# Performance work log

Hardware: AMD Instinct MI355X
Metric: run time of the kernel (lower is better)

## Reference

```python
import jax, jax.numpy as jnp
import numpy as np

B, S, D, H = 4, 2048, 1024, 16
DK = D // H
SCALE = float(np.sqrt(DK))
NEG_INF = jnp.float32(-1e30)


def setup_inputs() -> dict:
    key = jax.random.key(0)
    ks = jax.random.split(key, 12)
    std = 1.0 / np.sqrt(D)
    def lin(k):
        kw, kb = jax.random.split(k)
        W = jax.random.uniform(kw, (D, D), jnp.float32, -std, std)
        b = jax.random.uniform(kb, (D,), jnp.float32, -std, std)
        return W, b
    Wq, bq = lin(ks[0]); Wk, bk = lin(ks[1]); Wv, bv = lin(ks[2]); Wo, bo = lin(ks[3])
    query = jax.random.normal(ks[4], (B, S, D), jnp.float32)
    key_t = jax.random.normal(ks[5], (B, S, D), jnp.float32)
    value = jax.random.normal(ks[6], (B, S, D), jnp.float32)
    # causal mask, broadcastable to [B,H,S,S]; positions where mask==0 are blocked
    mask = jnp.tril(jnp.ones((S, S), dtype=bool))[None, None]
    return {"query": query, "key": key_t, "value": value,
            "Wq": Wq, "bq": bq, "Wk": Wk, "bk": bk, "Wv": Wv, "bv": bv,
            "Wo": Wo, "bo": bo, "mask": mask}


def reference(query, key, value, Wq, bq, Wk, bk, Wv, bv, Wo, bo, mask):
    # projections: x @ W.T + b (torch nn.Linear convention)
    q = (query @ Wq.T + bq).reshape(B, S, H, DK).transpose(0, 2, 1, 3)  # [B,H,S,DK]
    k = (key @ Wk.T + bk).reshape(B, S, H, DK).transpose(0, 2, 1, 3)
    v = (value @ Wv.T + bv).reshape(B, S, H, DK).transpose(0, 2, 1, 3)
    scores = jnp.einsum('bhqd,bhkd->bhqk', q, k) / SCALE  # [B,H,S,S]
    scores = jnp.where(mask, scores, NEG_INF)
    attn = jax.nn.softmax(scores, axis=-1)
    # dropout is identity in eval / p used at train only; omitted (p treated as 0)
    context = jnp.einsum('bhqk,bhkd->bhqd', attn, v)  # [B,H,S,DK]
    context = context.transpose(0, 2, 1, 3).reshape(B, S, D)
    return context @ Wo.T + bo
```

## Files before the change

### kernel.cpp

```cpp
#include <hip/hip_runtime.h>
#include <hip/hip_bf16.h>
#include <cstdint>
#include <cstddef>


namespace {

constexpr int B  = 4;
constexpr int S  = 2048;
constexpr int D  = 1024;
constexpr int H  = 16;
constexpr int DK = 64;
constexpr int M  = B * S;
constexpr float LOG2E     = 1.44269504088896f;
constexpr float QSCALE    = 0.125f * LOG2E;
constexpr float NEG_BIG   = -1e30f;
constexpr float DEFER_THR = 8.0f;

using bf16 = __hip_bfloat16;

typedef __attribute__((ext_vector_type(8))) __bf16 bf16x8;
typedef __attribute__((ext_vector_type(4))) float  f32x4;

__device__ __forceinline__ uint16_t f2bfu(float x) {
  uint32_t a = __builtin_bit_cast(uint32_t, x);
  return (uint16_t)((a + 0x7FFFu + ((a >> 16) & 1u)) >> 16);
}
__device__ __forceinline__ uint32_t pk2(float x, float y) {
  return (uint32_t)f2bfu(x) | ((uint32_t)f2bfu(y) << 16);
}
__device__ __forceinline__ float ex2(float x) {
  float r; asm("v_exp_f32 %0, %1" : "=v"(r) : "v"(x)); return r;
}
__device__ __forceinline__ uint32_t cvtpk(float lo, float hi) {
  uint32_t r;
  asm("v_cvt_pk_bf16_f32 %0, %1, %2" : "=v"(r) : "v"(lo), "v"(hi));
  return r;
}
__device__ __forceinline__ float hmax4(f32x4 v) {
  return fmaxf(fmaxf(v[0], v[1]), fmaxf(v[2], v[3]));
}

__device__ __forceinline__ void ldst16(const uint4* g, uint4* l) {
  __builtin_amdgcn_global_load_lds(
      (const __attribute__((address_space(1))) void*)g,
      (__attribute__((address_space(3))) void*)l, 16, 0, 0);
}

__device__ __forceinline__ void xcd_remap(int& bx, int& by) {
  const int orig = blockIdx.x + (blockIdx.y << 3);
  bx = (orig >> 3) & 7;
  by = ((orig & 7) << 3) + (orig >> 6);
}

__global__ __launch_bounds__(256)
void cvt_all(const float* __restrict__ q, const float* __restrict__ k,
             const float* __restrict__ v, const float* __restrict__ wq,
             const float* __restrict__ wk, const float* __restrict__ wv,
             const float* __restrict__ wo, bf16* __restrict__ dq,
             bf16* __restrict__ dk, bf16* __restrict__ dv,
             bf16* __restrict__ dw)
{
  constexpr int N8IN = 1 << 20;
  constexpr int N8W  = 1 << 17;
  constexpr int T3   = 3 * N8IN;

  const int gi = blockIdx.x * 256 + threadIdx.x;
  const float* src; bf16* dst; int i;
  if (gi < T3) {
    const int z = gi >> 20; i = gi & (N8IN - 1);
    src = (z == 0) ? q : (z == 1) ? k : v;
    dst = (z == 0) ? dq : (z == 1) ? dk : dv;
  } else {
    const int j = gi - T3;
    const int z = j >> 17; i = j & (N8W - 1);
    src = (z == 0) ? wq : (z == 1) ? wk : (z == 2) ? wv : wo;
    dst = dw + ((size_t)z << 20);
  }
  const float4 p = ((const float4*)src)[2 * i];
  const float4 r4 = ((const float4*)src)[2 * i + 1];
  uint4 r;
  r.x = pk2(p.x, p.y); r.y = pk2(p.z, p.w);
  r.z = pk2(r4.x, r4.y); r.w = pk2(r4.z, r4.w);
  ((uint4*)dst)[i] = r;
}

__global__ __launch_bounds__(256)
void cvt3(const float* __restrict__ a, const float* __restrict__ b,
          const float* __restrict__ c, bf16* __restrict__ x,
          bf16* __restrict__ y, bf16* __restrict__ z_, int n8)
{
  const int zz = blockIdx.y;
  const float* src = (zz == 0) ? a : (zz == 1) ? b : c;
  bf16*        dst = (zz == 0) ? x : (zz == 1) ? y : z_;
  const int i = blockIdx.x * 256 + threadIdx.x;
  if (i >= n8) return;
  const float4 p = ((const float4*)src)[2 * i];
  const float4 q = ((const float4*)src)[2 * i + 1];
  uint4 r;
  r.x = pk2(p.x, p.y); r.y = pk2(p.z, p.w);
  r.z = pk2(q.x, q.y); r.w = pk2(q.z, q.w);
  ((uint4*)dst)[i] = r;
}

__global__ __launch_bounds__(256, 4)
void proj_qkv(const bf16* __restrict__ Aq, const bf16* __restrict__ Ak,
              const bf16* __restrict__ Av, const bf16* __restrict__ Wall,
              const float* __restrict__ bq_, const float* __restrict__ bk_,
              const float* __restrict__ bv_, bf16* __restrict__ qo,
              bf16* __restrict__ ko, bf16* __restrict__ vto)
{
  __shared__ uint4 AsU[1024];
  __shared__ uint4 BsU[1024];

  const int z = blockIdx.z;
  const bf16*  A    = (z == 0) ? Aq : (z == 1) ? Ak : Av;
  const bf16*  Wb   = Wall + (size_t)z * D * D;
  const float* bias = (z == 0) ? bq_ : (z == 1) ? bk_ : bv_;

  const int tid  = threadIdx.x;
  const int w    = tid >> 6;
  const int lane = tid & 63;
  const int lm   = lane & 15;
  const int quad = lane >> 4;
  const int wm   = (w >> 1) * 64;
  const int wn   = (w & 1) * 64;

  int bx, by; xcd_remap(bx, by);
  const int row0 = by * 128, col0 = bx * 128;
  constexpr int g8 = D >> 3;

  const uint4* Ag = (const uint4*)A + (size_t)row0 * g8;
  const uint4* Bg = (const uint4*)Wb + (size_t)col0 * g8;

  f32x4 acc[4][4] = {};

  for (int kt = 0; kt < D / 64; ++kt) {
    __syncthreads();
#pragma unroll
    for (int i = 0; i < 4; ++i) {
      const int chunk = i * 256 + w * 64 + lane;
      const int r = chunk >> 3, c = chunk & 7;
      ldst16(&Ag[(size_t)r * g8 + kt * 8 + c], &AsU[i * 256 + w * 64]);
      ldst16(&Bg[(size_t)r * g8 + kt * 8 + c], &BsU[i * 256 + w * 64]);
    }
    __syncthreads();
#pragma unroll
    for (int kk = 0; kk < 2; ++kk) {
      bf16x8 af[4], bfr[4];
#pragma unroll
      for (int tm = 0; tm < 4; ++tm)
        af[tm] = __builtin_bit_cast(bf16x8, AsU[(wm + tm * 16 + lm) * 8 + kk * 4 + quad]);
#pragma unroll
      for (int tn = 0; tn < 4; ++tn)
        bfr[tn] = __builtin_bit_cast(bf16x8, BsU[(wn + tn * 16 + lm) * 8 + kk * 4 + quad]);
#pragma unroll
      for (int tm = 0; tm < 4; ++tm)
#pragma unroll
        for (int tn = 0; tn < 4; ++tn)
          acc[tm][tn] = __builtin_amdgcn_mfma_f32_16x16x32_bf16(af[tm], bfr[tn], acc[tm][tn], 0, 0, 0);
    }
  }

  const float scale = (z == 0) ? QSCALE : 1.0f;
#pragma unroll
  for (int tm = 0; tm < 4; ++tm) {
#pragma unroll
    for (int tn = 0; tn < 4; ++tn) {
      const int col = col0 + wn + tn * 16 + lm;
      const float bv = bias[col];
      if (z == 2) {
        float vv[4];
#pragma unroll
        for (int r = 0; r < 4; ++r) vv[r] = acc[tm][tn][r] + bv;
        const int s0 = row0 + wm + tm * 16 + quad * 4;
        const int b_ = s0 >> 11, ss = s0 & (S - 1);
        const int h_ = col >> 6, dk = col & (DK - 1);
        uint2 st; st.x = pk2(vv[0], vv[1]); st.y = pk2(vv[2], vv[3]);
        *(uint2*)(vto + (((size_t)b_ * H + h_) * DK + dk) * S + ss) = st;
      } else {
        bf16* out = (z == 0) ? qo : ko;
#pragma unroll
        for (int r = 0; r < 4; ++r) {
          const int row = row0 + wm + tm * 16 + quad * 4 + r;
          const float v = (acc[tm][tn][r] + bv) * scale;
          const int b_ = row >> 11, s_ = row & (S - 1);
          const int h_ = col >> 6,  dk = col & (DK - 1);
          out[(((size_t)b_ * H + h_) * S + s_) * DK + dk] =
              __builtin_bit_cast(bf16, f2bfu(v));
        }
      }
    }
  }
}

__global__ __launch_bounds__(512)
void gemm_out(const bf16* __restrict__ A, const bf16* __restrict__ Wb,
              const float* __restrict__ bias, float* __restrict__ out)
{
  __shared__ uint4 AsU[1024];
  __shared__ uint4 BsU[1024];

  const int tid  = threadIdx.x;
  const int w    = tid >> 6;
  const int lane = tid & 63;
  const int lm   = lane & 15;
  const int quad = lane >> 4;
  const int wm   = (w >> 2) * 64;
  const int wn   = (w & 3) * 32;

  int bx, by; xcd_remap(bx, by);
  const int row0 = by * 128, col0 = bx * 128;
  constexpr int g8 = D >> 3;

  const uint4* Ag = (const uint4*)A + (size_t)row0 * g8;
  const uint4* Bg = (const uint4*)Wb + (size_t)col0 * g8;

  f32x4 acc[4][2] = {};

  for (int kt = 0; kt < D / 64; ++kt) {
    __syncthreads();
#pragma unroll
    for (int i = 0; i < 2; ++i) {
      const int chunk = i * 512 + w * 64 + lane;
      const int r = chunk >> 3, c = chunk & 7;
      ldst16(&Ag[(size_t)r * g8 + kt * 8 + c], &AsU[i * 512 + w * 64]);
      ldst16(&Bg[(size_t)r * g8 + kt * 8 + c], &BsU[i * 512 + w * 64]);
    }
    __syncthreads();
#pragma unroll
    for (int kk = 0; kk < 2; ++kk) {
      bf16x8 af[4], bfr[2];
#pragma unroll
      for (int tm = 0; tm < 4; ++tm)
        af[tm] = __builtin_bit_cast(bf16x8, AsU[(wm + tm * 16 + lm) * 8 + kk * 4 + quad]);
#pragma unroll
      for (int tn = 0; tn < 2; ++tn)
        bfr[tn] = __builtin_bit_cast(bf16x8, BsU[(wn + tn * 16 + lm) * 8 + kk * 4 + quad]);
#pragma unroll
      for (int tm = 0; tm < 4; ++tm)
#pragma unroll
        for (int tn = 0; tn < 2; ++tn)
          acc[tm][tn] = __builtin_amdgcn_mfma_f32_16x16x32_bf16(af[tm], bfr[tn], acc[tm][tn], 0, 0, 0);
    }
  }

#pragma unroll
  for (int tm = 0; tm < 4; ++tm) {
#pragma unroll
    for (int tn = 0; tn < 2; ++tn) {
      const int col = col0 + wn + tn * 16 + lm;
      const float bv = bias[col];
#pragma unroll
      for (int r = 0; r < 4; ++r) {
        const int row = row0 + wm + tm * 16 + quad * 4 + r;
        out[(size_t)row * D + col] = acc[tm][tn][r] + bv;
      }
    }
  }
}

template <int MODE>
__global__ __launch_bounds__(256)
void gemm128(const bf16* __restrict__ A, const bf16* __restrict__ Wb,
             const float* __restrict__ bias, void* __restrict__ out,
             int N, int K, float scale)
{
  __shared__ uint4 AsU[2][1024];
  __shared__ uint4 BsU[2][1024];

  const int tid  = threadIdx.x;
  const int w    = tid >> 6;
  const int lane = tid & 63;
  const int lm   = lane & 15;
  const int quad = lane >> 4;
  const int wm   = (w >> 1) * 64;
  const int wn   = (w & 1) * 64;

  int bx, by; xcd_remap(bx, by);
  const int row0 = by * 128, col0 = bx * 128;
  const int g8 = K >> 3;

  const uint4* Ag = (const uint4*)A + (size_t)row0 * g8;
  const uint4* Bg = (const uint4*)Wb + (size_t)col0 * g8;

  f32x4 acc[4][4] = {};
  const int KT = K / 64;

#pragma unroll
  for (int i = 0; i < 4; ++i) {
    const int chunk = i * 256 + w * 64 + lane;
    const int r = chunk >> 3, c = chunk & 7;
    ldst16(&Ag[(size_t)r * g8 + c], &AsU[0][i * 256 + w * 64]);
    ldst16(&Bg[(size_t)r * g8 + c], &BsU[0][i * 256 + w * 64]);
  }

  int cur = 0;
  for (int kt = 0; kt < KT; ++kt) {
    __syncthreads();
    if (kt + 1 < KT) {
#pragma unroll
      for (int i = 0; i < 4; ++i) {
        const int chunk = i * 256 + w * 64 + lane;
        const int r = chunk >> 3, c = chunk & 7;
        ldst16(&Ag[(size_t)r * g8 + (kt + 1) * 8 + c], &AsU[cur ^ 1][i * 256 + w * 64]);
        ldst16(&Bg[(size_t)r * g8 + (kt + 1) * 8 + c], &BsU[cur ^ 1][i * 256 + w * 64]);
      }
    }
#pragma unroll
    for (int kk = 0; kk < 2; ++kk) {
      bf16x8 af[4], bfr[4];
#pragma unroll
      for (int tm = 0; tm < 4; ++tm)
        af[tm] = __builtin_bit_cast(bf16x8, AsU[cur][(wm + tm * 16 + lm) * 8 + kk * 4 + quad]);
#pragma unroll
      for (int tn = 0; tn < 4; ++tn)
        bfr[tn] = __builtin_bit_cast(bf16x8, BsU[cur][(wn + tn * 16 + lm) * 8 + kk * 4 + quad]);
#pragma unroll
      for (int tm = 0; tm < 4; ++tm)
#pragma unroll
        for (int tn = 0; tn < 4; ++tn)
          acc[tm][tn] = __builtin_amdgcn_mfma_f32_16x16x32_bf16(af[tm], bfr[tn], acc[tm][tn], 0, 0, 0);
    }
    cur ^= 1;
  }

#pragma unroll
  for (int tm = 0; tm < 4; ++tm) {
#pragma unroll
    for (int tn = 0; tn < 4; ++tn) {
      const int col = col0 + wn + tn * 16 + lm;
      const float bv = bias[col];
      if (MODE == 2) {
        float vv[4];
#pragma unroll
        for (int r = 0; r < 4; ++r) vv[r] = (acc[tm][tn][r] + bv) * scale;
        const int s0 = row0 + wm + tm * 16 + quad * 4;
        const int b_ = s0 >> 11, ss = s0 & (S - 1);
        const int h_ = col >> 6, dk = col & (DK - 1);
        uint2 st; st.x = pk2(vv[0], vv[1]); st.y = pk2(vv[2], vv[3]);
        *(uint2*)((bf16*)out + (((size_t)b_ * H + h_) * DK + dk) * S + ss) = st;
      } else {
#pragma unroll
        for (int r = 0; r < 4; ++r) {
          const int row = row0 + wm + tm * 16 + quad * 4 + r;
          const float v = (acc[tm][tn][r] + bv) * scale;
          if (MODE == 0) {
            ((float*)out)[(size_t)row * N + col] = v;
          } else {
            const int b_ = row >> 11, s_ = row & (S - 1);
            const int h_ = col >> 6,  dk = col & (DK - 1);
            ((bf16*)out)[(((size_t)b_ * H + h_) * S + s_) * DK + dk] =
                __builtin_bit_cast(bf16, f2bfu(v));
          }
        }
      }
    }
  }
}

__global__ __launch_bounds__(512)
void flash_mfma(const bf16* __restrict__ Q, const bf16* __restrict__ K,
                const bf16* __restrict__ Vt, bf16* __restrict__ ctx)
{
  __shared__ uint4 KsU[2][512];
  __shared__ uint4 VtU[2][512];
  __shared__ uint16_t Os[128 * 72];

  const int tid  = threadIdx.x;
  const int w    = tid >> 6;
  const int lane = tid & 63;
  const int lm   = lane & 15;
  const int quad = lane >> 4;
  const int bh   = blockIdx.x;
  const int pr   = blockIdx.y;
  const size_t base = (size_t)bh * S * DK;

  const uint4* Kg0 = (const uint4*)(K + base);
  const uint4* Vg0 = (const uint4*)(Vt + (size_t)bh * DK * S);

  const int rr  = w * 8 + (lane >> 3);
  const int csw = (lane & 7) ^ (lane >> 3) ^ ((w & 1) << 2);
  const int fv  = (lm & 7) ^ (((lm >> 3) & 1) << 2);
  const int r0  = ((lm >> 2) << 3) | (lm & 3);

  uint16_t* const Ow = Os + (w * 16) * 72;
  const int b_ = bh >> 4, h_ = bh & (H - 1);

  for (int pass = 0; pass < 2; ++pass) {
    const int qi = pass ? (15 - pr) : pr;
    const int q0 = qi * 128;
    const int qbase = q0 + w * 16;

    bf16x8 qf0, qf1;
    {
      const bf16* qrow = Q + base + (size_t)(qbase + lm) * DK;
      qf0 = __builtin_bit_cast(bf16x8, *(const uint4*)(qrow + quad * 8));
      qf1 = __builtin_bit_cast(bf16x8, *(const uint4*)(qrow + 32 + quad * 8));
    }

    f32x4 o[4] = {};
    float m_i = NEG_BIG, l_i = 0.f;

    const int nt = 2 * qi + 2;

    ldst16(&Kg0[(size_t)rr * 8 + csw],       &KsU[0][w * 64]);
    ldst16(&Vg0[(size_t)rr * (S / 8) + csw], &VtU[0][w * 64]);

    int cur = 0;
    for (int t = 0; t < nt; ++t) {
      __syncthreads();
      if (t + 1 < nt) {
        const int k1 = (t + 1) * 64;
        ldst16(&Kg0[(size_t)(k1 + rr) * 8 + csw],         &KsU[cur ^ 1][w * 64]);
        ldst16(&Vg0[(size_t)rr * (S / 8) + k1 / 8 + csw], &VtU[cur ^ 1][w * 64]);
      }
      const int k0 = t * 64;
      if (k0 <= qbase + 15) {
        const uint4* Ks = KsU[cur];
        const uint4* Vs = VtU[cur];

        f32x4 sc[4];
        __builtin_amdgcn_s_setprio(1);
#pragma unroll
        for (int tn = 0; tn < 4; ++tn) {
          const int row = r0 + ((tn & 1) << 2) + ((tn >> 1) << 5);
          const int fr  = (row & 7) ^ (((row >> 3) & 1) << 2);
          const int cb  = quad ^ fr;
          bf16x8 kb0 = __builtin_bit_cast(bf16x8, Ks[row * 8 + cb]);
          bf16x8 kb1 = __builtin_bit_cast(bf16x8, Ks[row * 8 + (cb ^ 4)]);
          sc[tn] = __builtin_amdgcn_mfma_f32_16x16x32_bf16(
                       kb0, qf0, f32x4{0.f, 0.f, 0.f, 0.f}, 0, 0, 0);
          sc[tn] = __builtin_amdgcn_mfma_f32_16x16x32_bf16(kb1, qf1, sc[tn], 0, 0, 0);
        }
        __builtin_amdgcn_s_setprio(0);

        if (k0 + 63 > qbase) {
          const int qg = qbase + lm;
#pragma unroll
          for (int tn = 0; tn < 4; ++tn) {
            const int kb_ = k0 + ((tn >> 1) << 5) + (quad << 3) + ((tn & 1) << 2);
#pragma unroll
            for (int r = 0; r < 4; ++r)
              if (kb_ + r > qg) sc[tn][r] = NEG_BIG;
          }
        }

        float mloc = fmaxf(fmaxf(hmax4(sc[0]), hmax4(sc[1])),
                           fmaxf(hmax4(sc[2]), hmax4(sc[3])));
        mloc = fmaxf(mloc, __shfl_xor(mloc, 16));
        mloc = fmaxf(mloc, __shfl_xor(mloc, 32));

        if (__any(mloc > m_i + DEFER_THR)) {
          const float mn = fmaxf(m_i, mloc);
          const float al = ex2(m_i - mn);
          l_i *= al; m_i = mn;
          const float a0 = __shfl(al, quad * 4 + 0, 16);
          const float a1 = __shfl(al, quad * 4 + 1, 16);
          const float a2 = __shfl(al, quad * 4 + 2, 16);
          const float a3 = __shfl(al, quad * 4 + 3, 16);
#pragma unroll
          for (int tn = 0; tn < 4; ++tn) {
            o[tn][0] *= a0; o[tn][1] *= a1; o[tn][2] *= a2; o[tn][3] *= a3;
          }
        }

        float ls = 0.f;
#pragma unroll
        for (int tn = 0; tn < 4; ++tn) {
#pragma unroll
          for (int r = 0; r < 4; ++r) sc[tn][r] = ex2(sc[tn][r] - m_i);
          ls += (sc[tn][0] + sc[tn][1]) + (sc[tn][2] + sc[tn][3]);
        }
        l_i += ls;

        uint4 pw0, pw1;
        pw0.x = cvtpk(sc[0][0], sc[0][1]); pw0.y = cvtpk(sc[0][2], sc[0][3]);
        pw0.z = cvtpk(sc[1][0], sc[1][1]); pw0.w = cvtpk(sc[1][2], sc[1][3]);
        pw1.x = cvtpk(sc[2][0], sc[2][1]); pw1.y = cvtpk(sc[2][2], sc[2][3]);
        pw1.z = cvtpk(sc[3][0], sc[3][1]); pw1.w = cvtpk(sc[3][2], sc[3][3]);
        const bf16x8 ap0 = __builtin_bit_cast(bf16x8, pw0);
        const bf16x8 ap1 = __builtin_bit_cast(bf16x8, pw1);

        __builtin_amdgcn_s_setprio(1);
#pragma unroll
        for (int tn = 0; tn < 4; ++tn) {
          const int vrow = tn * 16 + lm;
          const int cv = quad ^ fv;
          bf16x8 vb0 = __builtin_bit_cast(bf16x8, Vs[vrow * 8 + cv]);
          bf16x8 vb1 = __builtin_bit_cast(bf16x8, Vs[vrow * 8 + (cv ^ 4)]);
          o[tn] = __builtin_amdgcn_mfma_f32_16x16x32_bf16(ap0, vb0, o[tn], 0, 0, 0);
          o[tn] = __builtin_amdgcn_mfma_f32_16x16x32_bf16(ap1, vb1, o[tn], 0, 0, 0);
        }
        __builtin_amdgcn_s_setprio(0);
      }
      cur ^= 1;
    }

    __syncthreads();
    {
      float lr = l_i;
      lr += __shfl_xor(lr, 16);
      lr += __shfl_xor(lr, 32);
      const float inv = 1.f / lr;
      const float i0 = __shfl(inv, quad * 4 + 0, 16);
      const float i1 = __shfl(inv, quad * 4 + 1, 16);
      const float i2 = __shfl(inv, quad * 4 + 2, 16);
      const float i3 = __shfl(inv, quad * 4 + 3, 16);
#pragma unroll
      for (int tn = 0; tn < 4; ++tn) {
        Ow[(quad * 4 + 0) * 72 + tn * 16 + lm] = f2bfu(o[tn][0] * i0);
        Ow[(quad * 4 + 1) * 72 + tn * 16 + lm] = f2bfu(o[tn][1] * i1);
        Ow[(quad * 4 + 2) * 72 + tn * 16 + lm] = f2bfu(o[tn][2] * i2);
        Ow[(quad * 4 + 3) * 72 + tn * 16 + lm] = f2bfu(o[tn][3] * i3);
      }
    }
    __syncthreads();

#pragma unroll
    for (int i = 0; i < 2; ++i) {
      const int idx = tid + i * 512;
      const int row = idx >> 3, c = idx & 7;
      const uint4 v = *(const uint4*)(Os + row * 72 + c * 8);
      *(uint4*)(ctx + ((((size_t)b_ * S + q0 + row) * H + h_) << 6) + c * 8) = v;
    }
  }
}

}

extern "C" void kernel_launch(void* const* d_in, const int* in_sizes, int n_in,
                              void* d_out, int out_size, void* d_ws, size_t ws_size,
                              hipStream_t stream)
{
  const float* query = (const float*)d_in[0];
  const float* key_  = (const float*)d_in[1];
  const float* value = (const float*)d_in[2];
  const float* Wq    = (const float*)d_in[3];
  const float* bq    = (const float*)d_in[4];
  const float* Wk    = (const float*)d_in[5];
  const float* bk    = (const float*)d_in[6];
  const float* Wv    = (const float*)d_in[7];
  const float* bv    = (const float*)d_in[8];
  const float* Wo    = (const float*)d_in[9];
  const float* bo    = (const float*)d_in[10];

  const size_t qkv = (size_t)B * H * S * DK;
  const size_t DD  = (size_t)D * D;
  bf16* slot0 = (bf16*)d_ws;
  bf16* slot1 = slot0 + qkv;
  bf16* slot2 = slot1 + qkv;
  bf16* slot3 = slot2 + qkv;
  bf16* slot4 = slot3 + qkv;
  bf16* dout0 = (bf16*)d_out;
  bf16* dout1 = dout0 + qkv;

  const int n8in = (int)(qkv / 8);
  const int n8w  = (int)(DD / 8);
  const dim3 gproj(D / 128, M / 128);
  const dim3 gattn(B * H, 8);

  const size_t need = (4 * qkv + 4 * DD) * sizeof(bf16);

  if (ws_size >= need) {
    cvt_all<<<dim3((3 * n8in + 4 * n8w) / 256), 256, 0, stream>>>(
        query, key_, value, Wq, Wk, Wv, Wo, dout0, dout1, slot3, slot4);
    proj_qkv<<<dim3(D / 128, M / 128, 3), 256, 0, stream>>>(
        dout0, dout1, slot3, slot4, bq, bk, bv, slot0, slot1, slot2);
    flash_mfma<<<gattn, 512, 0, stream>>>(slot0, slot1, slot2, slot3);
    gemm_out<<<gproj, 512, 0, stream>>>(slot3, slot4 + 3 * DD, bo,
                                        (float*)d_out);
  } else {
    cvt3<<<dim3(n8in / 256, 3), 256, 0, stream>>>(query, key_, value,
                                                  dout0, dout1, slot3, n8in);
    cvt3<<<dim3(n8w / 256, 2), 256, 0, stream>>>(Wq, Wk, Wk,
                                                 slot2, slot2 + DD, slot2, n8w);
    gemm128<1><<<gproj, 256, 0, stream>>>(dout0, slot2, bq, slot0, D, D, QSCALE);
    gemm128<1><<<gproj, 256, 0, stream>>>(dout1, slot2 + DD, bk, slot1, D, D, 1.0f);
    cvt3<<<dim3(n8w / 256, 1), 256, 0, stream>>>(Wv, Wv, Wv,
                                                 dout0, dout0, dout0, n8w);
    gemm128<2><<<gproj, 256, 0, stream>>>(slot3, dout0, bv, slot2, D, D, 1.0f);
    flash_mfma<<<gattn, 512, 0, stream>>>(slot0, slot1, slot2, slot3);
    cvt3<<<dim3(n8w / 256, 1), 256, 0, stream>>>(Wo, Wo, Wo,
                                                 slot0, slot0, slot0, n8w);
    gemm128<0><<<gproj, 256, 0, stream>>>(slot3, slot0, bo, d_out, D, D, 1.0f);
  }
}
```

Baseline: 315.7 us.

## Pipeline projection GEMMs with triple-buffered LDS and 256x128 tiles

Rewrites the QKV projection and output GEMMs to use 256x128 block tiles with 512 threads and a three-stage LDS ring fed by async global-to-LDS loads, so the next tiles load while the current one computes. It XOR-swizzles the LDS layout to avoid bank conflicts, raises MFMA priority with setprio, and remaps blocks across XCDs for the new grid shape. The cost is much larger shared memory (144KB per block), which limits occupancy to one block per CU, and halves the number of blocks.

Result: slower. 325.9 us (+3.2%).

```diff
diff --git a/kernel.cpp b/kernel.cpp
--- a/kernel.cpp
+++ b/kernel.cpp
@@ -51,6 +51,13 @@
   const int orig = blockIdx.x + (blockIdx.y << 3);
   bx = (orig >> 3) & 7;
   by = ((orig & 7) << 3) + (orig >> 6);
+}
+
+__device__ __forceinline__ void xcd_remap256(int& bx, int& by) {
+  const int d = blockIdx.x + (blockIdx.y << 3);
+  const int j = d >> 3;
+  bx = j >> 2;
+  by = ((d & 7) << 2) | (j & 3);
 }
 
 __global__ __launch_bounds__(256)
@@ -103,15 +110,72 @@
   ((uint4*)dst)[i] = r;
 }
 
-__global__ __launch_bounds__(256, 4)
-void proj_qkv(const bf16* __restrict__ Aq, const bf16* __restrict__ Ak,
-              const bf16* __restrict__ Av, const bf16* __restrict__ Wall,
-              const float* __restrict__ bq_, const float* __restrict__ bk_,
-              const float* __restrict__ bv_, bf16* __restrict__ qo,
-              bf16* __restrict__ ko, bf16* __restrict__ vto)
+
+#define PIPE_STAGE(T, SL)                                                     \
+  {                                                                           \
+    const int kb = (T) * 8;                                                   \
+    _Pragma("unroll")                                                         \
+    for (int i = 0; i < 4; ++i)                                               \
+      ldst16(&Ag[(size_t)(i * 64 + rr) * 128 + kb + cs],                      \
+             &As[SL][i * 512 + (w << 6)]);                                    \
+    _Pragma("unroll")                                                         \
+    for (int i = 0; i < 2; ++i)                                               \
+      ldst16(&Bg[(size_t)(i * 64 + rr) * 128 + kb + cs],                      \
+             &Bs[SL][i * 512 + (w << 6)]);                                    \
+  }
+
+#define PIPE_LOOP()                                                           \
+  PIPE_STAGE(0, 0);                                                           \
+  PIPE_STAGE(1, 1);                                                           \
+  int s = 0;                                                                  \
+  for (int t = 0; t < 16; ++t) {                                              \
+    if (t < 15) asm volatile("s_waitcnt vmcnt(6)" ::: "memory");              \
+    else        asm volatile("s_waitcnt vmcnt(0)" ::: "memory");              \
+    __builtin_amdgcn_s_barrier();                                             \
+    __builtin_amdgcn_sched_barrier(0);                                        \
+    if (t + 2 < 16) {                                                         \
+      int s2 = s + 2; if (s2 >= 3) s2 -= 3;                                   \
+      PIPE_STAGE(t + 2, s2);                                                  \
+    }                                                                         \
+    const uint4* Asl = As[s];                                                 \
+    const uint4* Bsl = Bs[s];                                                 \
+    _Pragma("unroll")                                                         \
+    for (int qd = 0; qd < 4; ++qd) {                                          \
+      const int tm0 = (qd >> 1) * 2, tn0 = (qd & 1) * 2;                      \
+      bf16x8 a0[2], a1[2], b0[2], b1[2];                                      \
+      _Pragma("unroll")                                                       \
+      for (int x = 0; x < 2; ++x) {                                           \
+        const int ra = (wm + (tm0 + x) * 16 + lm) * 8;                        \
+        a0[x] = __builtin_bit_cast(bf16x8, Asl[ra + kc0]);                    \
+        a1[x] = __builtin_bit_cast(bf16x8, Asl[ra + (kc0 ^ 4)]);              \
+        const int rb = (wn + (tn0 + x) * 16 + lm) * 8;                        \
+        b0[x] = __builtin_bit_cast(bf16x8, Bsl[rb + kc0]);                    \
+        b1[x] = __builtin_bit_cast(bf16x8, Bsl[rb + (kc0 ^ 4)]);              \
+      }                                                                       \
+      __builtin_amdgcn_s_setprio(1);                                          \
+      _Pragma("unroll")                                                       \
+      for (int x = 0; x < 2; ++x)                                             \
+        _Pragma("unroll")                                                     \
+        for (int y = 0; y < 2; ++y) {                                         \
+          acc[tm0 + x][tn0 + y] = __builtin_amdgcn_mfma_f32_16x16x32_bf16(    \
+              a0[x], b0[y], acc[tm0 + x][tn0 + y], 0, 0, 0);                  \
+          acc[tm0 + x][tn0 + y] = __builtin_amdgcn_mfma_f32_16x16x32_bf16(    \
+              a1[x], b1[y], acc[tm0 + x][tn0 + y], 0, 0, 0);                  \
+        }                                                                     \
+      __builtin_amdgcn_s_setprio(0);                                          \
+    }                                                                         \
+    ++s; if (s == 3) s = 0;                                                   \
+  }
+
+__global__ __launch_bounds__(512)
+void proj_qkv8(const bf16* __restrict__ Aq, const bf16* __restrict__ Ak,
+               const bf16* __restrict__ Av, const bf16* __restrict__ Wall,
+               const float* __restrict__ bq_, const float* __restrict__ bk_,
+               const float* __restrict__ bv_, bf16* __restrict__ qo,
+               bf16* __restrict__ ko, bf16* __restrict__ vto)
 {
-  __shared__ uint4 AsU[1024];
-  __shared__ uint4 BsU[1024];
+  __shared__ uint4 As[3][2048];
+  __shared__ uint4 Bs[3][1024];
 
   const int z = blockIdx.z;
   const bf16*  A    = (z == 0) ? Aq : (z == 1) ? Ak : Av;
@@ -126,41 +190,19 @@
   const int wm   = (w >> 1) * 64;
   const int wn   = (w & 1) * 64;
 
-  int bx, by; xcd_remap(bx, by);
-  const int row0 = by * 128, col0 = bx * 128;
-  constexpr int g8 = D >> 3;
-
-  const uint4* Ag = (const uint4*)A + (size_t)row0 * g8;
-  const uint4* Bg = (const uint4*)Wb + (size_t)col0 * g8;
+  int bx, by; xcd_remap256(bx, by);
+  const int row0 = by * 256, col0 = bx * 128;
+
+  const uint4* Ag = (const uint4*)A + (size_t)row0 * 128;
+  const uint4* Bg = (const uint4*)Wb + (size_t)col0 * 128;
+
+  const int rr = (w << 3) + (lane >> 3);
+  const int cs = (lane & 7) ^ (lane >> 3);
+  const int kc0 = quad ^ (lm & 7);
 
   f32x4 acc[4][4] = {};
 
-  for (int kt = 0; kt < D / 64; ++kt) {
-    __syncthreads();
-#pragma unroll
-    for (int i = 0; i < 4; ++i) {
-      const int chunk = i * 256 + w * 64 + lane;
-      const int r = chunk >> 3, c = chunk & 7;
-      ldst16(&Ag[(size_t)r * g8 + kt * 8 + c], &AsU[i * 256 + w * 64]);
-      ldst16(&Bg[(size_t)r * g8 + kt * 8 + c], &BsU[i * 256 + w * 64]);
-    }
-    __syncthreads();
-#pragma unroll
-    for (int kk = 0; kk < 2; ++kk) {
-      bf16x8 af[4], bfr[4];
-#pragma unroll
-      for (int tm = 0; tm < 4; ++tm)
-        af[tm] = __builtin_bit_cast(bf16x8, AsU[(wm + tm * 16 + lm) * 8 + kk * 4 + quad]);
-#pragma unroll
-      for (int tn = 0; tn < 4; ++tn)
-        bfr[tn] = __builtin_bit_cast(bf16x8, BsU[(wn + tn * 16 + lm) * 8 + kk * 4 + quad]);
-#pragma unroll
-      for (int tm = 0; tm < 4; ++tm)
-#pragma unroll
-        for (int tn = 0; tn < 4; ++tn)
-          acc[tm][tn] = __builtin_amdgcn_mfma_f32_16x16x32_bf16(af[tm], bfr[tn], acc[tm][tn], 0, 0, 0);
-    }
-  }
+  PIPE_LOOP();
 
   const float scale = (z == 0) ? QSCALE : 1.0f;
 #pragma unroll
@@ -195,60 +237,38 @@
 }
 
 __global__ __launch_bounds__(512)
-void gemm_out(const bf16* __restrict__ A, const bf16* __restrict__ Wb,
-              const float* __restrict__ bias, float* __restrict__ out)
+void gemm_out8(const bf16* __restrict__ A, const bf16* __restrict__ Wb,
+               const float* __restrict__ bias, float* __restrict__ out)
 {
-  __shared__ uint4 AsU[1024];
-  __shared__ uint4 BsU[1024];
+  __shared__ uint4 As[3][2048];
+  __shared__ uint4 Bs[3][1024];
 
   const int tid  = threadIdx.x;
   const int w    = tid >> 6;
   const int lane = tid & 63;
   const int lm   = lane & 15;
   const int quad = lane >> 4;
-  const int wm   = (w >> 2) * 64;
-  const int wn   = (w & 3) * 32;
-
-  int bx, by; xcd_remap(bx, by);
-  const int row0 = by * 128, col0 = bx * 128;
-  constexpr int g8 = D >> 3;
-
-  const uint4* Ag = (const uint4*)A + (size_t)row0 * g8;
-  const uint4* Bg = (const uint4*)Wb + (size_t)col0 * g8;
-
-  f32x4 acc[4][2] = {};
-
-  for (int kt = 0; kt < D / 64; ++kt) {
-    __syncthreads();
-#pragma unroll
-    for (int i = 0; i < 2; ++i) {
-      const int chunk = i * 512 + w * 64 + lane;
-      const int r = chunk >> 3, c = chunk & 7;
-      ldst16(&Ag[(size_t)r * g8 + kt * 8 + c], &AsU[i * 512 + w * 64]);
-      ldst16(&Bg[(size_t)r * g8 + kt * 8 + c], &BsU[i * 512 + w * 64]);
-    }
-    __syncthreads();
-#pragma unroll
-    for (int kk = 0; kk < 2; ++kk) {
-      bf16x8 af[4], bfr[2];
-#pragma unroll
-      for (int tm = 0; tm < 4; ++tm)
-        af[tm] = __builtin_bit_cast(bf16x8, AsU[(wm + tm * 16 + lm) * 8 + kk * 4 + quad]);
-#pragma unroll
-      for (int tn = 0; tn < 2; ++tn)
-        bfr[tn] = __builtin_bit_cast(bf16x8, BsU[(wn + tn * 16 + lm) * 8 + kk * 4 + quad]);
-#pragma unroll
-      for (int tm = 0; tm < 4; ++tm)
-#pragma unroll
-        for (int tn = 0; tn < 2; ++tn)
-          acc[tm][tn] = __builtin_amdgcn_mfma_f32_16x16x32_bf16(af[tm], bfr[tn], acc[tm][tn], 0, 0, 0);
-    }
-  }
+  const int wm   = (w >> 1) * 64;
+  const int wn   = (w & 1) * 64;
+
+  int bx, by; xcd_remap256(bx, by);
+  const int row0 = by * 256, col0 = bx * 128;
+
+  const uint4* Ag = (const uint4*)A + (size_t)row0 * 128;
+  const uint4* Bg = (const uint4*)Wb + (size_t)col0 * 128;
+
+  const int rr = (w << 3) + (lane >> 3);
+  const int cs = (lane & 7) ^ (lane >> 3);
+  const int kc0 = quad ^ (lm & 7);
+
+  f32x4 acc[4][4] = {};
+
+  PIPE_LOOP();
 
 #pragma unroll
   for (int tm = 0; tm < 4; ++tm) {
 #pragma unroll
-    for (int tn = 0; tn < 2; ++tn) {
+    for (int tn = 0; tn < 4; ++tn) {
       const int col = col0 + wn + tn * 16 + lm;
       const float bv = bias[col];
 #pragma unroll
@@ -565,11 +585,11 @@
   if (ws_size >= need) {
     cvt_all<<<dim3((3 * n8in + 4 * n8w) / 256), 256, 0, stream>>>(
         query, key_, value, Wq, Wk, Wv, Wo, dout0, dout1, slot3, slot4);
-    proj_qkv<<<dim3(D / 128, M / 128, 3), 256, 0, stream>>>(
+    proj_qkv8<<<dim3(8, 32, 3), 512, 0, stream>>>(
         dout0, dout1, slot3, slot4, bq, bk, bv, slot0, slot1, slot2);
     flash_mfma<<<gattn, 512, 0, stream>>>(slot0, slot1, slot2, slot3);
-    gemm_out<<<gproj, 512, 0, stream>>>(slot3, slot4 + 3 * DD, bo,
-                                        (float*)d_out);
+    gemm_out8<<<dim3(8, 32), 512, 0, stream>>>(slot3, slot4 + 3 * DD, bo,
+                                               (float*)d_out);
   } else {
     cvt3<<<dim3(n8in / 256, 3), 256, 0, stream>>>(query, key_, value,
                                                   dout0, dout1, slot3, n8in);
```

## Give each attention wave two 16-row query groups with 256-thread blocks

Applied to the files above, without the earlier changes.

The flash attention kernel drops from 8 waves of 16 query rows each to 4 waves of 32 query rows each (two 16-row groups per wave). Each K/V fragment read from LDS is now reused across two MFMA row groups, which halves LDS reads per unit of compute, and each thread issues twice as many global-to-LDS loads. The cost is doubled per-wave register state (two score tiles, two output accumulators, two softmax states) and fewer waves per block to hide latency. Causal skipping is kept per 16-row group.

After: 332.4 us. +5.3%, slower.

```diff
diff --git a/kernel.cpp b/kernel.cpp
--- a/kernel.cpp
+++ b/kernel.cpp
@@ -359,7 +359,7 @@
   }
 }
 
-__global__ __launch_bounds__(512)
+__global__ __launch_bounds__(256)
 void flash_mfma(const bf16* __restrict__ Q, const bf16* __restrict__ K,
                 const bf16* __restrict__ Vt, bf16* __restrict__ ctx)
 {
@@ -379,48 +379,54 @@
   const uint4* Kg0 = (const uint4*)(K + base);
   const uint4* Vg0 = (const uint4*)(Vt + (size_t)bh * DK * S);
 
-  const int rr  = w * 8 + (lane >> 3);
-  const int csw = (lane & 7) ^ (lane >> 3) ^ ((w & 1) << 2);
+  const int rr  = tid >> 3;
+  const int csw = (tid & 7) ^ ((tid >> 3) & 7) ^ (((tid >> 6) & 1) << 2);
   const int fv  = (lm & 7) ^ (((lm >> 3) & 1) << 2);
   const int r0  = ((lm >> 2) << 3) | (lm & 3);
 
-  uint16_t* const Ow = Os + (w * 16) * 72;
   const int b_ = bh >> 4, h_ = bh & (H - 1);
 
   for (int pass = 0; pass < 2; ++pass) {
     const int qi = pass ? (15 - pr) : pr;
     const int q0 = qi * 128;
-    const int qbase = q0 + w * 16;
-
-    bf16x8 qf0, qf1;
-    {
-      const bf16* qrow = Q + base + (size_t)(qbase + lm) * DK;
-      qf0 = __builtin_bit_cast(bf16x8, *(const uint4*)(qrow + quad * 8));
-      qf1 = __builtin_bit_cast(bf16x8, *(const uint4*)(qrow + 32 + quad * 8));
-    }
-
-    f32x4 o[4] = {};
-    float m_i = NEG_BIG, l_i = 0.f;
+    const int qb = q0 + w * 32;
+
+    bf16x8 qf[2][2];
+#pragma unroll
+    for (int g = 0; g < 2; ++g) {
+      const bf16* qrow = Q + base + (size_t)(qb + g * 16 + lm) * DK;
+      qf[g][0] = __builtin_bit_cast(bf16x8, *(const uint4*)(qrow + quad * 8));
+      qf[g][1] = __builtin_bit_cast(bf16x8, *(const uint4*)(qrow + 32 + quad * 8));
+    }
+
+    f32x4 o[2][4] = {};
+    float m_i[2] = {NEG_BIG, NEG_BIG};
+    float l_i[2] = {0.f, 0.f};
 
     const int nt = 2 * qi + 2;
 
-    ldst16(&Kg0[(size_t)rr * 8 + csw],       &KsU[0][w * 64]);
-    ldst16(&Vg0[(size_t)rr * (S / 8) + csw], &VtU[0][w * 64]);
+    ldst16(&Kg0[(size_t)rr * 8 + csw],               &KsU[0][w * 64]);
+    ldst16(&Kg0[(size_t)(32 + rr) * 8 + csw],        &KsU[0][256 + w * 64]);
+    ldst16(&Vg0[(size_t)rr * (S / 8) + csw],         &VtU[0][w * 64]);
+    ldst16(&Vg0[(size_t)(32 + rr) * (S / 8) + csw],  &VtU[0][256 + w * 64]);
 
     int cur = 0;
     for (int t = 0; t < nt; ++t) {
       __syncthreads();
       if (t + 1 < nt) {
         const int k1 = (t + 1) * 64;
-        ldst16(&Kg0[(size_t)(k1 + rr) * 8 + csw],         &KsU[cur ^ 1][w * 64]);
-        ldst16(&Vg0[(size_t)rr * (S / 8) + k1 / 8 + csw], &VtU[cur ^ 1][w * 64]);
+        ldst16(&Kg0[(size_t)(k1 + rr) * 8 + csw],               &KsU[cur ^ 1][w * 64]);
+        ldst16(&Kg0[(size_t)(k1 + 32 + rr) * 8 + csw],          &KsU[cur ^ 1][256 + w * 64]);
+        ldst16(&Vg0[(size_t)rr * (S / 8) + k1 / 8 + csw],       &VtU[cur ^ 1][w * 64]);
+        ldst16(&Vg0[(size_t)(32 + rr) * (S / 8) + k1 / 8 + csw], &VtU[cur ^ 1][256 + w * 64]);
       }
       const int k0 = t * 64;
-      if (k0 <= qbase + 15) {
+      if (k0 <= qb + 31) {
+        const bool a0 = (k0 <= qb + 15);
         const uint4* Ks = KsU[cur];
         const uint4* Vs = VtU[cur];
 
-        f32x4 sc[4];
+        f32x4 sc[2][4];
         __builtin_amdgcn_s_setprio(1);
 #pragma unroll
         for (int tn = 0; tn < 4; ++tn) {
@@ -429,58 +435,70 @@
           const int cb  = quad ^ fr;
           bf16x8 kb0 = __builtin_bit_cast(bf16x8, Ks[row * 8 + cb]);
           bf16x8 kb1 = __builtin_bit_cast(bf16x8, Ks[row * 8 + (cb ^ 4)]);
-          sc[tn] = __builtin_amdgcn_mfma_f32_16x16x32_bf16(
-                       kb0, qf0, f32x4{0.f, 0.f, 0.f, 0.f}, 0, 0, 0);
-          sc[tn] = __builtin_amdgcn_mfma_f32_16x16x32_bf16(kb1, qf1, sc[tn], 0, 0, 0);
+          sc[1][tn] = __builtin_amdgcn_mfma_f32_16x16x32_bf16(
+                          kb0, qf[1][0], f32x4{0.f, 0.f, 0.f, 0.f}, 0, 0, 0);
+          sc[1][tn] = __builtin_amdgcn_mfma_f32_16x16x32_bf16(kb1, qf[1][1], sc[1][tn], 0, 0, 0);
+          if (a0) {
+            sc[0][tn] = __builtin_amdgcn_mfma_f32_16x16x32_bf16(
+                            kb0, qf[0][0], f32x4{0.f, 0.f, 0.f, 0.f}, 0, 0, 0);
+            sc[0][tn] = __builtin_amdgcn_mfma_f32_16x16x32_bf16(kb1, qf[0][1], sc[0][tn], 0, 0, 0);
+          }
         }
         __builtin_amdgcn_s_setprio(0);
 
-        if (k0 + 63 > qbase) {
-          const int qg = qbase + lm;
+        bf16x8 ap[2][2];
+#pragma unroll
+        for (int g = 0; g < 2; ++g) {
+          if (g == 0 && !a0) continue;
+          const int qbg = qb + g * 16;
+          if (k0 + 63 > qbg) {
+            const int qg = qbg + lm;
+#pragma unroll
+            for (int tn = 0; tn < 4; ++tn) {
+              const int kb_ = k0 + ((tn >> 1) << 5) + (quad << 3) + ((tn & 1) << 2);
+#pragma unroll
+              for (int r = 0; r < 4; ++r)
+                if (kb_ + r > qg) sc[g][tn][r] = NEG_BIG;
+            }
+          }
+
+          float mloc = fmaxf(fmaxf(hmax4(sc[g][0]), hmax4(sc[g][1])),
+                             fmaxf(hmax4(sc[g][2]), hmax4(sc[g][3])));
+          mloc = fmaxf(mloc, __shfl_xor(mloc, 16));
+          mloc = fmaxf(mloc, __shfl_xor(mloc, 32));
+
+          if (__any(mloc > m_i[g] + DEFER_THR)) {
+            const float mn = fmaxf(m_i[g], mloc);
+            const float al = ex2(m_i[g] - mn);
+            l_i[g] *= al; m_i[g] = mn;
+            const float a0_ = __shfl(al, quad * 4 + 0, 16);
+            const float a1_ = __shfl(al, quad * 4 + 1, 16);
+            const float a2_ = __shfl(al, quad * 4 + 2, 16);
+            const float a3_ = __shfl(al, quad * 4 + 3, 16);
+#pragma unroll
+            for (int tn = 0; tn < 4; ++tn) {
+              o[g][tn][0] *= a0_; o[g][tn][1] *= a1_;
+              o[g][tn][2] *= a2_; o[g][tn][3] *= a3_;
+            }
+          }
+
+          float ls = 0.f;
 #pragma unroll
           for (int tn = 0; tn < 4; ++tn) {
-            const int kb_ = k0 + ((tn >> 1) << 5) + (quad << 3) + ((tn & 1) << 2);
-#pragma unroll
-            for (int r = 0; r < 4; ++r)
-              if (kb_ + r > qg) sc[tn][r] = NEG_BIG;
+#pragma unroll
+            for (int r = 0; r < 4; ++r) sc[g][tn][r] = ex2(sc[g][tn][r] - m_i[g]);
+            ls += (sc[g][tn][0] + sc[g][tn][1]) + (sc[g][tn][2] + sc[g][tn][3]);
           }
+          l_i[g] += ls;
+
+          uint4 pw0, pw1;
+          pw0.x = cvtpk(sc[g][0][0], sc[g][0][1]); pw0.y = cvtpk(sc[g][0][2], sc[g][0][3]);
+          pw0.z = cvtpk(sc[g][1][0], sc[g][1][1]); pw0.w = cvtpk(sc[g][1][2], sc[g][1][3]);
+          pw1.x = cvtpk(sc[g][2][0], sc[g][2][1]); pw1.y = cvtpk(sc[g][2][2], sc[g][2][3]);
+          pw1.z = cvtpk(sc[g][3][0], sc[g][3][1]); pw1.w = cvtpk(sc[g][3][2], sc[g][3][3]);
+          ap[g][0] = __builtin_bit_cast(bf16x8, pw0);
+          ap[g][1] = __builtin_bit_cast(bf16x8, pw1);
         }
-
-        float mloc = fmaxf(fmaxf(hmax4(sc[0]), hmax4(sc[1])),
-                           fmaxf(hmax4(sc[2]), hmax4(sc[3])));
-        mloc = fmaxf(mloc, __shfl_xor(mloc, 16));
-        mloc = fmaxf(mloc, __shfl_xor(mloc, 32));
-
-        if (__any(mloc > m_i + DEFER_THR)) {
-          const float mn = fmaxf(m_i, mloc);
-          const float al = ex2(m_i - mn);
-          l_i *= al; m_i = mn;
-          const float a0 = __shfl(al, quad * 4 + 0, 16);
-          const float a1 = __shfl(al, quad * 4 + 1, 16);
-          const float a2 = __shfl(al, quad * 4 + 2, 16);
-          const float a3 = __shfl(al, quad * 4 + 3, 16);
-#pragma unroll
-          for (int tn = 0; tn < 4; ++tn) {
-            o[tn][0] *= a0; o[tn][1] *= a1; o[tn][2] *= a2; o[tn][3] *= a3;
-          }
-        }
-
-        float ls = 0.f;
-#pragma unroll
-        for (int tn = 0; tn < 4; ++tn) {
-#pragma unroll
-          for (int r = 0; r < 4; ++r) sc[tn][r] = ex2(sc[tn][r] - m_i);
-          ls += (sc[tn][0] + sc[tn][1]) + (sc[tn][2] + sc[tn][3]);
-        }
-        l_i += ls;
-
-        uint4 pw0, pw1;
-        pw0.x = cvtpk(sc[0][0], sc[0][1]); pw0.y = cvtpk(sc[0][2], sc[0][3]);
-        pw0.z = cvtpk(sc[1][0], sc[1][1]); pw0.w = cvtpk(sc[1][2], sc[1][3]);
-        pw1.x = cvtpk(sc[2][0], sc[2][1]); pw1.y = cvtpk(sc[2][2], sc[2][3]);
-        pw1.z = cvtpk(sc[3][0], sc[3][1]); pw1.w = cvtpk(sc[3][2], sc[3][3]);
-        const bf16x8 ap0 = __builtin_bit_cast(bf16x8, pw0);
-        const bf16x8 ap1 = __builtin_bit_cast(bf16x8, pw1);
 
         __builtin_amdgcn_s_setprio(1);
 #pragma unroll
@@ -489,8 +507,12 @@
           const int cv = quad ^ fv;
           bf16x8 vb0 = __builtin_bit_cast(bf16x8, Vs[vrow * 8 + cv]);
           bf16x8 vb1 = __builtin_bit_cast(bf16x8, Vs[vrow * 8 + (cv ^ 4)]);
-          o[tn] = __builtin_amdgcn_mfma_f32_16x16x32_bf16(ap0, vb0, o[tn], 0, 0, 0);
-          o[tn] = __builtin_amdgcn_mfma_f32_16x16x32_bf16(ap1, vb1, o[tn], 0, 0, 0);
+          o[1][tn] = __builtin_amdgcn_mfma_f32_16x16x32_bf16(ap[1][0], vb0, o[1][tn], 0, 0, 0);
+          o[1][tn] = __builtin_amdgcn_mfma_f32_16x16x32_bf16(ap[1][1], vb1, o[1][tn], 0, 0, 0);
+          if (a0) {
+            o[0][tn] = __builtin_amdgcn_mfma_f32_16x16x32_bf16(ap[0][0], vb0, o[0][tn], 0, 0, 0);
+            o[0][tn] = __builtin_amdgcn_mfma_f32_16x16x32_bf16(ap[0][1], vb1, o[0][tn], 0, 0, 0);
+          }
         }
         __builtin_amdgcn_s_setprio(0);
       }
@@ -498,8 +520,10 @@
     }
 
     __syncthreads();
-    {
-      float lr = l_i;
+#pragma unroll
+    for (int g = 0; g < 2; ++g) {
+      uint16_t* const Ow = Os + (w * 32 + g * 16) * 72;
+      float lr = l_i[g];
       lr += __shfl_xor(lr, 16);
       lr += __shfl_xor(lr, 32);
       const float inv = 1.f / lr;
@@ -509,17 +533,17 @@
       const float i3 = __shfl(inv, quad * 4 + 3, 16);
 #pragma unroll
       for (int tn = 0; tn < 4; ++tn) {
-        Ow[(quad * 4 + 0) * 72 + tn * 16 + lm] = f2bfu(o[tn][0] * i0);
-        Ow[(quad * 4 + 1) * 72 + tn * 16 + lm] = f2bfu(o[tn][1] * i1);
-        Ow[(quad * 4 + 2) * 72 + tn * 16 + lm] = f2bfu(o[tn][2] * i2);
-        Ow[(quad * 4 + 3) * 72 + tn * 16 + lm] = f2bfu(o[tn][3] * i3);
+        Ow[(quad * 4 + 0) * 72 + tn * 16 + lm] = f2bfu(o[g][tn][0] * i0);
+        Ow[(quad * 4 + 1) * 72 + tn * 16 + lm] = f2bfu(o[g][tn][1] * i1);
+        Ow[(quad * 4 + 2) * 72 + tn * 16 + lm] = f2bfu(o[g][tn][2] * i2);
+        Ow[(quad * 4 + 3) * 72 + tn * 16 + lm] = f2bfu(o[g][tn][3] * i3);
       }
     }
     __syncthreads();
 
 #pragma unroll
-    for (int i = 0; i < 2; ++i) {
-      const int idx = tid + i * 512;
+    for (int i = 0; i < 4; ++i) {
+      const int idx = tid + i * 256;
       const int row = idx >> 3, c = idx & 7;
       const uint4 v = *(const uint4*)(Os + row * 72 + c * 8);
       *(uint4*)(ctx + ((((size_t)b_ * S + q0 + row) * H + h_) << 6) + c * 8) = v;
@@ -567,7 +591,7 @@
         query, key_, value, Wq, Wk, Wv, Wo, dout0, dout1, slot3, slot4);
     proj_qkv<<<dim3(D / 128, M / 128, 3), 256, 0, stream>>>(
         dout0, dout1, slot3, slot4, bq, bk, bv, slot0, slot1, slot2);
-    flash_mfma<<<gattn, 512, 0, stream>>>(slot0, slot1, slot2, slot3);
+    flash_mfma<<<gattn, 256, 0, stream>>>(slot0, slot1, slot2, slot3);
     gemm_out<<<gproj, 512, 0, stream>>>(slot3, slot4 + 3 * DD, bo,
                                         (float*)d_out);
   } else {
@@ -580,7 +604,7 @@
     cvt3<<<dim3(n8w / 256, 1), 256, 0, stream>>>(Wv, Wv, Wv,
                                                  dout0, dout0, dout0, n8w);
     gemm128<2><<<gproj, 256, 0, stream>>>(slot3, dout0, bv, slot2, D, D, 1.0f);
-    flash_mfma<<<gattn, 512, 0, stream>>>(slot0, slot1, slot2, slot3);
+    flash_mfma<<<gattn, 256, 0, stream>>>(slot0, slot1, slot2, slot3);
     cvt3<<<dim3(n8w / 256, 1), 256, 0, stream>>>(Wo, Wo, Wo,
                                                  slot0, slot0, slot0, n8w);
     gemm128<0><<<gproj, 256, 0, stream>>>(slot3, slot0, bo, d_out, D, D, 1.0f);
```
